# Kernel tuning notes

Measured on AMD Instinct MI355X. Metric: run time of the kernel, lower is better.

## Reference

```python
import jax, jax.numpy as jnp
import numpy as np

N_LIG, M_POC = 16384, 32768
E_LIG, E_POC, K_CROSS = 163840, 327680, 8
H = 64
L = 4

silu = jax.nn.silu


def _lin(k, fan_in, fan_out):
    k1, k2 = jax.random.split(k)
    s = 1.0 / np.sqrt(fan_in)
    W = jax.random.uniform(k1, (fan_in, fan_out), jnp.float32, -s, s)
    b = jax.random.uniform(k2, (fan_out,), jnp.float32, -s, s)
    return W, b


def setup_inputs() -> dict:
    key = jax.random.key(0)
    ks = jax.random.split(key, 32)
    inp = {
        'lig_x': jax.random.normal(ks[0], (N_LIG, 3), jnp.float32),
        'lig_h': jax.random.normal(ks[1], (N_LIG, 17), jnp.float32),
        'poc_x': jax.random.normal(ks[2], (M_POC, 3), jnp.float32),
        'poc_h': jax.random.normal(ks[3], (M_POC, 29), jnp.float32),
        'lig_edge_index': jax.random.randint(ks[4], (2, E_LIG), 0, N_LIG, jnp.int32),
        'lig_edge_attr': jax.random.normal(ks[5], (E_LIG, 6), jnp.float32),
        'poc_edge_index': jax.random.randint(ks[6], (2, E_POC), 0, M_POC, jnp.int32),
        'poc_edge_attr': jax.random.normal(ks[7], (E_POC, 16), jnp.float32),
        'cross_edge_index': jnp.stack([
            jax.random.randint(ks[8], (N_LIG * K_CROSS,), 0, M_POC, jnp.int32),
            jax.random.randint(ks[9], (N_LIG * K_CROSS,), 0, N_LIG, jnp.int32)]),
        'cross_edge_attr': jax.random.normal(ks[10], (N_LIG * K_CROSS, 16), jnp.float32),
        't': jax.random.uniform(ks[11], (1,), jnp.float32),
    }
    # embeddings
    inp['lig_emb_W'], inp['lig_emb_b'] = _lin(ks[12], 18, H)
    inp['poc_emb_W'], inp['poc_emb_b'] = _lin(ks[13], 29, H)
    inp['lig_ee_W'], inp['lig_ee_b'] = _lin(ks[14], 6, H)
    inp['poc_ee_W'], inp['poc_ee_b'] = _lin(ks[15], 16, H)
    inp['cross_ee_W'], inp['cross_ee_b'] = _lin(ks[16], 16, H)
    # per-layer params stacked along leading L axis
    def stack(kk, fan_in, fan_out):
        Ws, bs = zip(*[_lin(k, fan_in, fan_out) for k in jax.random.split(kk, L)])
        return jnp.stack(Ws), jnp.stack(bs)
    inp['phi_e_W1'], inp['phi_e_b1'] = stack(ks[17], 2 * H + 1 + H, H)
    inp['phi_e_W2'], inp['phi_e_b2'] = stack(ks[18], H, H)
    inp['phi_x_W1'], inp['phi_x_b1'] = stack(ks[19], H, H)
    inp['phi_x_W2'], inp['phi_x_b2'] = stack(ks[20], H, 1)
    inp['phi_h_W1'], inp['phi_h_b1'] = stack(ks[21], 2 * H, H)
    inp['phi_h_W2'], inp['phi_h_b2'] = stack(ks[22], H, H)
    inp['out_W1'], inp['out_b1'] = _lin(ks[23], H, H)
    inp['out_W2'], inp['out_b2'] = _lin(ks[24], H, 1)
    return inp


def _forward(lig_x, lig_h, poc_x, poc_h, lig_edge_attr, poc_edge_attr,
             cross_edge_attr, t,
             lig_emb_W, lig_emb_b, poc_emb_W, poc_emb_b,
             lig_ee_W, lig_ee_b, poc_ee_W, poc_ee_b, cross_ee_W, cross_ee_b,
             phi_e_W1, phi_e_b1, phi_e_W2, phi_e_b2,
             phi_x_W1, phi_x_b1, phi_x_W2, phi_x_b2,
             phi_h_W1, phi_h_b1, phi_h_W2, phi_h_b2,
             out_W1, out_b1, out_W2, out_b2,
             lig_edge_index, poc_edge_index, cross_edge_index):
    n_lig = lig_h.shape[0]
    n_tot = n_lig + poc_h.shape[0]
    t_feat = jnp.broadcast_to(t.reshape(1, 1), (n_lig, 1))
    h_lig = jnp.concatenate([lig_h, t_feat], -1) @ lig_emb_W + lig_emb_b
    h_poc = poc_h @ poc_emb_W + poc_emb_b
    h = jnp.concatenate([h_lig, h_poc], 0)          # [N, H]
    x = jnp.concatenate([lig_x, poc_x], 0)          # [N, 3]
    src = jnp.concatenate([lig_edge_index[0], poc_edge_index[0] + n_lig,
                           cross_edge_index[0] + n_lig])
    dst = jnp.concatenate([lig_edge_index[1], poc_edge_index[1] + n_lig,
                           cross_edge_index[1]])
    eattr = jnp.concatenate([
        lig_edge_attr @ lig_ee_W + lig_ee_b,
        poc_edge_attr @ poc_ee_W + poc_ee_b,
        cross_edge_attr @ cross_ee_W + cross_ee_b], 0)  # [E, H]
    # True = pocket => coords not updated
    update_mask = jnp.concatenate([
        jnp.ones((n_lig, 1), h.dtype), jnp.zeros((n_tot - n_lig, 1), h.dtype)], 0)
    for i in range(phi_e_W1.shape[0]):
        diff = x[src] - x[dst]                                    # [E, 3]
        dist = jnp.sum(diff * diff, -1, keepdims=True) / 100.0    # [E, 1]
        e_in = jnp.concatenate([h[src], h[dst], dist, eattr], -1) # [E, 2H+1+H]
        m = silu(silu(e_in @ phi_e_W1[i] + phi_e_b1[i]) @ phi_e_W2[i] + phi_e_b2[i])
        cw = jnp.tanh(silu(m @ phi_x_W1[i] + phi_x_b1[i]) @ phi_x_W2[i] + phi_x_b2[i])
        coord_agg = jax.ops.segment_sum(diff * cw, dst, num_segments=n_tot) * update_mask
        msg_agg = jax.ops.segment_sum(m, dst, num_segments=n_tot)
        h = h + silu(jnp.concatenate([h, msg_agg], -1) @ phi_h_W1[i] + phi_h_b1[i]) @ phi_h_W2[i] + phi_h_b2[i]
        x = x + coord_agg
    disp = x[:n_lig] - lig_x
    scale = silu(h[:n_lig] @ out_W1 + out_b1) @ out_W2 + out_b2
    return scale * disp


def reference(lig_x, lig_h, poc_x, poc_h, lig_edge_attr, poc_edge_attr,
              cross_edge_attr, t,
              lig_emb_W, lig_emb_b, poc_emb_W, poc_emb_b,
              lig_ee_W, lig_ee_b, poc_ee_W, poc_ee_b, cross_ee_W, cross_ee_b,
              phi_e_W1, phi_e_b1, phi_e_W2, phi_e_b2,
              phi_x_W1, phi_x_b1, phi_x_W2, phi_x_b2,
              phi_h_W1, phi_h_b1, phi_h_W2, phi_h_b2,
              out_W1, out_b1, out_W2, out_b2,
              lig_edge_index, poc_edge_index, cross_edge_index):
    return _forward(lig_x, lig_h, poc_x, poc_h, lig_edge_attr, poc_edge_attr,
                    cross_edge_attr, t,
                    lig_emb_W, lig_emb_b, poc_emb_W, poc_emb_b,
                    lig_ee_W, lig_ee_b, poc_ee_W, poc_ee_b, cross_ee_W, cross_ee_b,
                    phi_e_W1, phi_e_b1, phi_e_W2, phi_e_b2,
                    phi_x_W1, phi_x_b1, phi_x_W2, phi_x_b2,
                    phi_h_W1, phi_h_b1, phi_h_W2, phi_h_b2,
                    out_W1, out_b1, out_W2, out_b2,
                    lig_edge_index, poc_edge_index, cross_edge_index)
```

## Files before the change

### kernel.cpp

```cpp
#include <hip/hip_runtime.h>

#define N_LIG 16384
#define M_POC 32768
#define N_TOT (N_LIG + M_POC)
#define E_LIG 163840
#define E_POC 327680
#define E_CROSS (N_LIG * 8)
#define E_TOT (E_LIG + E_POC + E_CROSS)
#define TE 16

typedef __bf16 bf16_t;
typedef bf16_t bf16x8 __attribute__((ext_vector_type(8)));
typedef bf16_t bf16x4 __attribute__((ext_vector_type(4)));
typedef float f32x4 __attribute__((ext_vector_type(4)));

#define SM 72
#define EDGE_WAVE_BYTES (32 * SM * 2)

__device__ __forceinline__ float fast_rcp(float x) { return __builtin_amdgcn_rcpf(x); }
__device__ __forceinline__ float silu_f(float v) {
    return v * fast_rcp(1.0f + __expf(-v));
}
__device__ __forceinline__ float tanh_f(float v) {
    float a = fabsf(v);
    float t = __expf(-2.0f * a);
    float r = (1.0f - t) * fast_rcp(1.0f + t);
    return copysignf(r, v);
}

__device__ __forceinline__ void atomic_add_f32(float* p, float v) {
    __hip_atomic_fetch_add(p, v, __ATOMIC_RELAXED, __HIP_MEMORY_SCOPE_AGENT);
}

__device__ __forceinline__ void lds_fence() {
    asm volatile("s_waitcnt lgkmcnt(0)" ::: "memory");
}


__global__ void k_build_edges(const int* __restrict__ lig_ei, const int* __restrict__ poc_ei,
                              const int* __restrict__ cross_ei,
                              int* __restrict__ srcA, int* __restrict__ dstA,
                              int* __restrict__ cnt) {
    int e = blockIdx.x * blockDim.x + threadIdx.x;
    if (e >= E_TOT) return;
    int s, d;
    if (e < E_LIG) {
        s = lig_ei[e];
        d = lig_ei[E_LIG + e];
    } else if (e < E_LIG + E_POC) {
        int i = e - E_LIG;
        s = poc_ei[i] + N_LIG;
        d = poc_ei[E_POC + i] + N_LIG;
    } else {
        int i = e - E_LIG - E_POC;
        s = cross_ei[i] + N_LIG;
        d = cross_ei[E_CROSS + i];
    }
    srcA[e] = s;
    dstA[e] = d;
    atomicAdd(&cnt[d], 1);
}

__global__ __launch_bounds__(1024) void k_scan(const int* __restrict__ cnt,
                                               int* __restrict__ rowptr,
                                               int* __restrict__ cursor) {
    __shared__ int sums[1024];
    int tid = threadIdx.x;
    int local[48];
    int s = 0;
    for (int i = 0; i < 48; ++i) { local[i] = s; s += cnt[tid * 48 + i]; }
    sums[tid] = s;
    __syncthreads();
    for (int off = 1; off < 1024; off <<= 1) {
        int v = (tid >= off) ? sums[tid - off] : 0;
        __syncthreads();
        sums[tid] += v;
        __syncthreads();
    }
    int base = (tid == 0) ? 0 : sums[tid - 1];
    for (int i = 0; i < 48; ++i) {
        int v = base + local[i];
        int idx = tid * 48 + i;
        rowptr[idx] = v;
        cursor[idx] = v;
    }
    if (tid == 1023) rowptr[N_TOT] = sums[1023];
}

__global__ void k_scatter(const int* __restrict__ dstA, int* __restrict__ cursor,
                          int* __restrict__ sortedPos) {
    int e = blockIdx.x * blockDim.x + threadIdx.x;
    if (e < E_TOT) sortedPos[e] = atomicAdd(&cursor[dstA[e]], 1);
}

#define PK_G1   (12 * 5 * 4 * 64)
#define PK_G23  (4 * 4 * 4 * 64)
#define PK_WH   (4 * 24 * 64)
#define PK_BEFF (12 * 64)
#define PK_TOT  (PK_G1 + PK_G23 + PK_WH + PK_BEFF)

__global__ void k_pack_all(const float* __restrict__ phi_e_W1, const float* __restrict__ phi_e_b1,
                           const float* __restrict__ lig_ee_W, const float* __restrict__ lig_ee_b,
                           const float* __restrict__ poc_ee_W, const float* __restrict__ poc_ee_b,
                           const float* __restrict__ cross_ee_W, const float* __restrict__ cross_ee_b,
                           const float* __restrict__ phi_e_W2, const float* __restrict__ phi_x_W1,
                           const float* __restrict__ phi_h_W1, const float* __restrict__ phi_h_W2,
                           bf16_t* __restrict__ Bg1, bf16_t* __restrict__ Bg23,
                           bf16_t* __restrict__ WhP, float* __restrict__ beff) {
    int tid = blockIdx.x * blockDim.x + threadIdx.x;
    if (tid < PK_G1) {
        int lt = tid / 1280;
        int rem = tid - lt * 1280;
        int c = rem >> 8;
        int ft = (rem >> 6) & 3;
        int lane = rem & 63;
        int l = lt / 3, t = lt % 3;
        const float* W1l = phi_e_W1 + l * 193 * 64;
        const float* We; int K;
        if (t == 0) { We = lig_ee_W; K = 6; }
        else if (t == 1) { We = poc_ee_W; K = 16; }
        else { We = cross_ee_W; K = 16; }
        int col = ft * 16 + (lane & 15);
        int k0 = c * 32 + (lane >> 4) * 8;
        #pragma unroll
        for (int j = 0; j < 8; ++j) {
            int row = k0 + j;
            float v = 0.0f;
            if (row < 128) v = W1l[row * 64 + col];
            else if (row < 144) {
                int kk = row - 128;
                if (kk < K) {
                    float a = 0.0f;
                    for (int q = 0; q < 64; ++q) a = fmaf(We[kk * 64 + q], W1l[(129 + q) * 64 + col], a);
                    v = a;
                }
            } else if (row == 144) {
                v = W1l[128 * 64 + col];
            }
            Bg1[(size_t)tid * 8 + j] = (bf16_t)v;
        }
    } else if (tid < PK_G1 + PK_G23) {
        int u = tid - PK_G1;
        int lane = u & 63;
        int ft = (u >> 6) & 3;
        int c = (u >> 8) & 3;
        int l = u >> 10;
        const float* W = (c < 2) ? (phi_e_W2 + l * 4096) : (phi_x_W1 + l * 4096);
        int kb = (c & 1) * 32;
        int col = ft * 16 + (lane & 15);
        int k0 = kb + (lane >> 4) * 8;
        #pragma unroll
        for (int j = 0; j < 8; ++j)
            Bg23[(size_t)u * 8 + j] = (bf16_t)W[(k0 + j) * 64 + col];
    } else if (tid < PK_G1 + PK_G23 + PK_WH) {
        int u = tid - PK_G1 - PK_G23;
        int lane = u & 63;
        int frag = (u >> 6) % 24;
        int l = (u >> 6) / 24;
        const float* W; int kc, ft;
        if (frag < 16) { W = phi_h_W1 + l * 128 * 64; kc = frag >> 2; ft = frag & 3; }
        else           { W = phi_h_W2 + l * 64 * 64;  kc = (frag - 16) >> 2; ft = (frag - 16) & 3; }
        int col = ft * 16 + (lane & 15);
        int k0 = kc * 32 + (lane >> 4) * 8;
        #pragma unroll
        for (int j = 0; j < 8; ++j)
            WhP[(size_t)u * 8 + j] = (bf16_t)W[(k0 + j) * 64 + col];
    } else if (tid < PK_TOT) {
        int u = tid - PK_G1 - PK_G23 - PK_WH;
        int j = u & 63;
        int lt = u >> 6;
        int l = lt / 3, t = lt % 3;
        const float* W1l = phi_e_W1 + l * 193 * 64;
        const float* Be = (t == 0) ? lig_ee_b : ((t == 1) ? poc_ee_b : cross_ee_b);
        float v = phi_e_b1[l * 64 + j];
        for (int q = 0; q < 64; ++q) v = fmaf(Be[q], W1l[(129 + q) * 64 + j], v);
        beff[u] = v;
    }
}

__global__ void k_embed(const float* __restrict__ lig_x, const float* __restrict__ lig_h,
                        const float* __restrict__ poc_x, const float* __restrict__ poc_h,
                        const float* __restrict__ t,
                        const float* __restrict__ ligW, const float* __restrict__ ligB,
                        const float* __restrict__ pocW, const float* __restrict__ pocB,
                        float* __restrict__ h, bf16_t* __restrict__ hB, float* __restrict__ x4) {
    int gid = blockIdx.x * blockDim.x + threadIdx.x;
    int n = gid >> 6;
    int lane = gid & 63;
    if (n >= N_TOT) return;
    float a;
    if (n < N_LIG) {
        a = ligB[lane];
        #pragma unroll
        for (int k = 0; k < 17; ++k) a = fmaf(lig_h[n * 17 + k], ligW[k * 64 + lane], a);
        a = fmaf(t[0], ligW[17 * 64 + lane], a);
        if (lane < 4) x4[n * 4 + lane] = (lane < 3) ? lig_x[n * 3 + lane] : 0.0f;
    } else {
        int p = n - N_LIG;
        a = pocB[lane];
        #pragma unroll
        for (int k = 0; k < 29; ++k) a = fmaf(poc_h[p * 29 + k], pocW[k * 64 + lane], a);
        if (lane < 4) x4[n * 4 + lane] = (lane < 3) ? poc_x[p * 3 + lane] : 0.0f;
    }
    h[n * 64 + lane] = a;
    hB[n * 64 + lane] = (bf16_t)a;
}

__global__ __launch_bounds__(256, 4) void k_edge_mfma(
    const bf16_t* __restrict__ hB, const float* __restrict__ x4,
    const int* __restrict__ srcA, const int* __restrict__ dstA,
    const int* __restrict__ sortedPos,
    const float* __restrict__ lig_attr, const float* __restrict__ poc_attr,
    const float* __restrict__ cross_attr,
    const bf16_t* __restrict__ Bg1L,
    const float* __restrict__ beffL,
    const bf16_t* __restrict__ Bg23L,
    const float* __restrict__ b2, const float* __restrict__ bx1,
    const float* __restrict__ Wx2, const float* __restrict__ bx2,
    bf16_t* __restrict__ mBuf, float* __restrict__ coord_agg) {
    __shared__ __align__(16) char lds[4 * EDGE_WAVE_BYTES];
    const int lane = threadIdx.x & 63;
    const int wave = threadIdx.x >> 6;
    bf16_t* mT = (bf16_t*)(lds + wave * EDGE_WAVE_BYTES);
    const int base = (blockIdx.x * 4 + wave) * 32;

    int tt; const float* attrBase; int astride;
    if (base < E_LIG) { tt = 0; attrBase = lig_attr + (size_t)base * 6; astride = 6; }
    else if (base < E_LIG + E_POC) { tt = 1; attrBase = poc_attr + (size_t)(base - E_LIG) * 16; astride = 16; }
    else { tt = 2; attrBase = cross_attr + (size_t)(base - E_LIG - E_POC) * 16; astride = 16; }

    const int edge = lane & 15;
    const int kgrp = lane >> 4;
    const int mrow0 = kgrp * 4;
    const int e0 = base + edge;
    const int e1 = base + 16 + edge;
    const int sv0 = srcA[e0], sv1 = srcA[e1];
    const int dv0 = dstA[e0], dv1 = dstA[e1];
    const int sp0 = sortedPos[e0], sp1 = sortedPos[e1];

    bf16x8 hs0a = *(const bf16x8*)(hB + (size_t)sv0 * 64 + kgrp * 8);
    bf16x8 hs0b = *(const bf16x8*)(hB + (size_t)sv0 * 64 + 32 + kgrp * 8);
    bf16x8 hd0a = *(const bf16x8*)(hB + (size_t)dv0 * 64 + kgrp * 8);
    bf16x8 hd0b = *(const bf16x8*)(hB + (size_t)dv0 * 64 + 32 + kgrp * 8);
    bf16x8 hs1a = *(const bf16x8*)(hB + (size_t)sv1 * 64 + kgrp * 8);
    bf16x8 hs1b = *(const bf16x8*)(hB + (size_t)sv1 * 64 + 32 + kgrp * 8);
    bf16x8 hd1a = *(const bf16x8*)(hB + (size_t)dv1 * 64 + kgrp * 8);
    bf16x8 hd1b = *(const bf16x8*)(hB + (size_t)dv1 * 64 + 32 + kgrp * 8);

    const bf16_t Z = (bf16_t)0.0f;
    bf16x8 ex0 = {Z, Z, Z, Z, Z, Z, Z, Z};
    bf16x8 ex1 = {Z, Z, Z, Z, Z, Z, Z, Z};
    float d0s0 = 0.f, d1s0 = 0.f, d2s0 = 0.f;
    float d0s1 = 0.f, d1s1 = 0.f, d2s1 = 0.f;
    if (kgrp == 0) {
        const float* a0p = attrBase + (size_t)edge * astride;
        const float* a1p = attrBase + (size_t)(16 + edge) * astride;
        if (tt == 0) {
            float4 q0 = *(const float4*)a0p;
            float2 q1 = *(const float2*)(a0p + 4);
            ex0 = (bf16x8){(bf16_t)q0.x, (bf16_t)q0.y, (bf16_t)q0.z, (bf16_t)q0.w,
                           (bf16_t)q1.x, (bf16_t)q1.y, Z, Z};
            float4 r0 = *(const float4*)a1p;
            float2 r1 = *(const float2*)(a1p + 4);
            ex1 = (bf16x8){(bf16_t)r0.x, (bf16_t)r0.y, (bf16_t)r0.z, (bf16_t)r0.w,
                           (bf16_t)r1.x, (bf16_t)r1.y, Z, Z};
        } else {
            float4 q0 = *(const float4*)a0p;
            float4 q1 = *(const float4*)(a0p + 4);
            ex0 = (bf16x8){(bf16_t)q0.x, (bf16_t)q0.y, (bf16_t)q0.z, (bf16_t)q0.w,
                           (bf16_t)q1.x, (bf16_t)q1.y, (bf16_t)q1.z, (bf16_t)q1.w};
            float4 r0 = *(const float4*)a1p;
            float4 r1 = *(const float4*)(a1p + 4);
            ex1 = (bf16x8){(bf16_t)r0.x, (bf16_t)r0.y, (bf16_t)r0.z, (bf16_t)r0.w,
                           (bf16_t)r1.x, (bf16_t)r1.y, (bf16_t)r1.z, (bf16_t)r1.w};
        }
    } else if (kgrp == 1) {
        if (tt != 0) {
            const float* a0p = attrBase + (size_t)edge * astride + 8;
            const float* a1p = attrBase + (size_t)(16 + edge) * astride + 8;
            float4 q0 = *(const float4*)a0p;
            float4 q1 = *(const float4*)(a0p + 4);
            ex0 = (bf16x8){(bf16_t)q0.x, (bf16_t)q0.y, (bf16_t)q0.z, (bf16_t)q0.w,
                           (bf16_t)q1.x, (bf16_t)q1.y, (bf16_t)q1.z, (bf16_t)q1.w};
            float4 r0 = *(const float4*)a1p;
            float4 r1 = *(const float4*)(a1p + 4);
            ex1 = (bf16x8){(bf16_t)r0.x, (bf16_t)r0.y, (bf16_t)r0.z, (bf16_t)r0.w,
                           (bf16_t)r1.x, (bf16_t)r1.y, (bf16_t)r1.z, (bf16_t)r1.w};
        }
    } else if (kgrp == 2) {
        float4 xs0 = *(const float4*)(x4 + (size_t)sv0 * 4);
        float4 xd0 = *(const float4*)(x4 + (size_t)dv0 * 4);
        float4 xs1 = *(const float4*)(x4 + (size_t)sv1 * 4);
        float4 xd1 = *(const float4*)(x4 + (size_t)dv1 * 4);
        d0s0 = xs0.x - xd0.x; d1s0 = xs0.y - xd0.y; d2s0 = xs0.z - xd0.z;
        d0s1 = xs1.x - xd1.x; d1s1 = xs1.y - xd1.y; d2s1 = xs1.z - xd1.z;
        float dist0 = (d0s0 * d0s0 + d1s0 * d1s0 + d2s0 * d2s0) * 0.01f;
        float dist1 = (d0s1 * d0s1 + d1s1 * d1s1 + d2s1 * d2s1) * 0.01f;
        ex0[0] = (bf16_t)dist0;
        ex1[0] = (bf16_t)dist1;
    }

    const bf16_t* Bg1 = Bg1L + (size_t)tt * 5 * 4 * 512;
    const float* beff = beffL + tt * 64;
    f32x4 acc0[4], acc1[4];
    #pragma unroll
    for (int ft = 0; ft < 4; ++ft) {
        float4 bv = *(const float4*)(beff + ft * 16 + mrow0);
        acc0[ft] = (f32x4){bv.x, bv.y, bv.z, bv.w};
        acc1[ft] = acc0[ft];
    }
    bf16x8 bdat0[5] = {hs0a, hs0b, hd0a, hd0b, ex0};
    bf16x8 bdat1[5] = {hs1a, hs1b, hd1a, hd1b, ex1};
    #pragma unroll
    for (int c = 0; c < 5; ++c) {
        #pragma unroll
        for (int ft = 0; ft < 4; ++ft) {
            bf16x8 wfr = *(const bf16x8*)(Bg1 + ((size_t)(c * 4 + ft) * 64 + lane) * 8);
            acc0[ft] = __builtin_amdgcn_mfma_f32_16x16x32_bf16(wfr, bdat0[c], acc0[ft], 0, 0, 0);
            acc1[ft] = __builtin_amdgcn_mfma_f32_16x16x32_bf16(wfr, bdat1[c], acc1[ft], 0, 0, 0);
        }
    }
    #pragma unroll
    for (int ft = 0; ft < 4; ++ft) {
        bf16x4 v0 = {(bf16_t)silu_f(acc0[ft][0]), (bf16_t)silu_f(acc0[ft][1]),
                     (bf16_t)silu_f(acc0[ft][2]), (bf16_t)silu_f(acc0[ft][3])};
        bf16x4 v1 = {(bf16_t)silu_f(acc1[ft][0]), (bf16_t)silu_f(acc1[ft][1]),
                     (bf16_t)silu_f(acc1[ft][2]), (bf16_t)silu_f(acc1[ft][3])};
        *(bf16x4*)(mT + edge * SM + ft * 16 + mrow0) = v0;
        *(bf16x4*)(mT + (16 + edge) * SM + ft * 16 + mrow0) = v1;
    }
    lds_fence();

    f32x4 acc20[4], acc21[4];
    #pragma unroll
    for (int ft = 0; ft < 4; ++ft) {
        float4 bv = *(const float4*)(b2 + ft * 16 + mrow0);
        acc20[ft] = (f32x4){bv.x, bv.y, bv.z, bv.w};
        acc21[ft] = acc20[ft];
    }
    bf16x8 m10[2], m11[2];
    #pragma unroll
    for (int c = 0; c < 2; ++c) {
        m10[c] = *(const bf16x8*)(mT + edge * SM + c * 32 + kgrp * 8);
        m11[c] = *(const bf16x8*)(mT + (16 + edge) * SM + c * 32 + kgrp * 8);
    }
    #pragma unroll
    for (int c = 0; c < 2; ++c) {
        #pragma unroll
        for (int ft = 0; ft < 4; ++ft) {
            bf16x8 wfr = *(const bf16x8*)(Bg23L + ((size_t)(c * 4 + ft) * 64 + lane) * 8);
            acc20[ft] = __builtin_amdgcn_mfma_f32_16x16x32_bf16(wfr, m10[c], acc20[ft], 0, 0, 0);
            acc21[ft] = __builtin_amdgcn_mfma_f32_16x16x32_bf16(wfr, m11[c], acc21[ft], 0, 0, 0);
        }
    }
    lds_fence();
    #pragma unroll
    for (int ft = 0; ft < 4; ++ft) {
        bf16x4 v0 = {(bf16_t)silu_f(acc20[ft][0]), (bf16_t)silu_f(acc20[ft][1]),
                     (bf16_t)silu_f(acc20[ft][2]), (bf16_t)silu_f(acc20[ft][3])};
        bf16x4 v1 = {(bf16_t)silu_f(acc21[ft][0]), (bf16_t)silu_f(acc21[ft][1]),
                     (bf16_t)silu_f(acc21[ft][2]), (bf16_t)silu_f(acc21[ft][3])};
        *(bf16x4*)(mT + edge * SM + ft * 16 + mrow0) = v0;
        *(bf16x4*)(mT + (16 + edge) * SM + ft * 16 + mrow0) = v1;
    }
    lds_fence();

    bf16x8 g0[2], g1[2];
    #pragma unroll
    for (int c = 0; c < 2; ++c) {
        g0[c] = *(const bf16x8*)(mT + edge * SM + c * 32 + kgrp * 8);
        g1[c] = *(const bf16x8*)(mT + (16 + edge) * SM + c * 32 + kgrp * 8);
        *(bf16x8*)(mBuf + (size_t)sp0 * 64 + c * 32 + kgrp * 8) = g0[c];
        *(bf16x8*)(mBuf + (size_t)sp1 * 64 + c * 32 + kgrp * 8) = g1[c];
    }

    f32x4 acc30[4], acc31[4];
    #pragma unroll
    for (int ft = 0; ft < 4; ++ft) {
        float4 bv = *(const float4*)(bx1 + ft * 16 + mrow0);
        acc30[ft] = (f32x4){bv.x, bv.y, bv.z, bv.w};
        acc31[ft] = acc30[ft];
    }
    const bf16_t* Bg3 = Bg23L + (size_t)2 * 4 * 512;
    #pragma unroll
    for (int c = 0; c < 2; ++c) {
        #pragma unroll
        for (int ft = 0; ft < 4; ++ft) {
            bf16x8 wfr = *(const bf16x8*)(Bg3 + ((size_t)(c * 4 + ft) * 64 + lane) * 8);
            acc30[ft] = __builtin_amdgcn_mfma_f32_16x16x32_bf16(wfr, g0[c], acc30[ft], 0, 0, 0);
            acc31[ft] = __builtin_amdgcn_mfma_f32_16x16x32_bf16(wfr, g1[c], acc31[ft], 0, 0, 0);
        }
    }

    float s0 = 0.0f, s1 = 0.0f;
    #pragma unroll
    for (int ft = 0; ft < 4; ++ft) {
        float4 wv = *(const float4*)(Wx2 + ft * 16 + mrow0);
        s0 = fmaf(silu_f(acc30[ft][0]), wv.x, s0);
        s0 = fmaf(silu_f(acc30[ft][1]), wv.y, s0);
        s0 = fmaf(silu_f(acc30[ft][2]), wv.z, s0);
        s0 = fmaf(silu_f(acc30[ft][3]), wv.w, s0);
        s1 = fmaf(silu_f(acc31[ft][0]), wv.x, s1);
        s1 = fmaf(silu_f(acc31[ft][1]), wv.y, s1);
        s1 = fmaf(silu_f(acc31[ft][2]), wv.z, s1);
        s1 = fmaf(silu_f(acc31[ft][3]), wv.w, s1);
    }
    s0 += __shfl_xor(s0, 16, 64); s0 += __shfl_xor(s0, 32, 64);
    s1 += __shfl_xor(s1, 16, 64); s1 += __shfl_xor(s1, 32, 64);
    const float bx2v = bx2[0];
    const float cw0 = tanh_f(s0 + bx2v);
    const float cw1 = tanh_f(s1 + bx2v);

    float a0 = __shfl(d0s0, 32 + edge, 64);
    float a1 = __shfl(d1s0, 32 + edge, 64);
    float a2 = __shfl(d2s0, 32 + edge, 64);
    float b0 = __shfl(d0s1, 32 + edge, 64);
    float b1 = __shfl(d1s1, 32 + edge, 64);
    float b2v_ = __shfl(d2s1, 32 + edge, 64);
    if (kgrp < 3) {
        float dsel0 = (kgrp == 0) ? a0 : ((kgrp == 1) ? a1 : a2);
        float dsel1 = (kgrp == 0) ? b0 : ((kgrp == 1) ? b1 : b2v_);
        if (dv0 < N_LIG) atomic_add_f32(&coord_agg[dv0 * 3 + kgrp], dsel0 * cw0);
        if (dv1 < N_LIG) atomic_add_f32(&coord_agg[dv1 * 3 + kgrp], dsel1 * cw1);
    }
}

#define NODE_WAVE_BYTES (2304 + 2304)
__global__ __launch_bounds__(256) void k_node(
    float* __restrict__ h, bf16_t* __restrict__ hB, float* __restrict__ x4,
    const bf16_t* __restrict__ mBuf, const int* __restrict__ rowptr,
    float* __restrict__ coord,
    const bf16_t* __restrict__ WhL,
    const float* __restrict__ bh1, const float* __restrict__ bh2) {
    __shared__ __align__(16) char lds[4 * NODE_WAVE_BYTES];
    const int lane = threadIdx.x & 63;
    const int wave = threadIdx.x >> 6;
    bf16_t* msgT = (bf16_t*)(lds + wave * NODE_WAVE_BYTES);
    bf16_t* mid  = (bf16_t*)(lds + wave * NODE_WAVE_BYTES + 2304);
    const int base = (blockIdx.x * 4 + wave) * TE;

    const int node = lane & 15;
    const int kgrp = lane >> 4;
    const int mrow0 = kgrp * 4;
    const int n16 = base + node;

    const int rp0 = rowptr[n16];
    const int rp1 = rowptr[n16 + 1];
    const int f4 = node * 4;
    for (int r = 0; r < TE; ++r) {
        const int s0 = __shfl(rp0, r, 64);
        const int s1 = __shfl(rp1, r, 64);
        float a0 = 0.f, a1 = 0.f, a2 = 0.f, a3 = 0.f;
        for (int i = s0 + kgrp; i < s1; i += 4) {
            bf16x4 v = *(const bf16x4*)(mBuf + (size_t)i * 64 + f4);
            a0 += (float)v[0]; a1 += (float)v[1]; a2 += (float)v[2]; a3 += (float)v[3];
        }
        a0 += __shfl_xor(a0, 16, 64); a1 += __shfl_xor(a1, 16, 64);
        a2 += __shfl_xor(a2, 16, 64); a3 += __shfl_xor(a3, 16, 64);
        a0 += __shfl_xor(a0, 32, 64); a1 += __shfl_xor(a1, 32, 64);
        a2 += __shfl_xor(a2, 32, 64); a3 += __shfl_xor(a3, 32, 64);
        if (lane < 16) {
            bf16x4 v = {(bf16_t)a0, (bf16_t)a1, (bf16_t)a2, (bf16_t)a3};
            *(bf16x4*)(msgT + r * SM + f4) = v;
        }
    }
    lds_fence();

    f32x4 acc[4];
    #pragma unroll
    for (int ft = 0; ft < 4; ++ft) {
        float4 bv = *(const float4*)(bh1 + ft * 16 + mrow0);
        acc[ft] = (f32x4){bv.x, bv.y, bv.z, bv.w};
    }
    bf16x8 d0 = *(const bf16x8*)(hB + (size_t)n16 * 64 + kgrp * 8);
    bf16x8 d1 = *(const bf16x8*)(hB + (size_t)n16 * 64 + 32 + kgrp * 8);
    bf16x8 d2 = *(const bf16x8*)(msgT + node * SM + kgrp * 8);
    bf16x8 d3 = *(const bf16x8*)(msgT + node * SM + 32 + kgrp * 8);
    bf16x8 bdat[4] = {d0, d1, d2, d3};
    #pragma unroll
    for (int c = 0; c < 4; ++c) {
        #pragma unroll
        for (int ft = 0; ft < 4; ++ft) {
            bf16x8 wfr = *(const bf16x8*)(WhL + ((size_t)(c * 4 + ft) * 64 + lane) * 8);
            acc[ft] = __builtin_amdgcn_mfma_f32_16x16x32_bf16(wfr, bdat[c], acc[ft], 0, 0, 0);
        }
    }
    #pragma unroll
    for (int ft = 0; ft < 4; ++ft) {
        bf16x4 v = {(bf16_t)silu_f(acc[ft][0]), (bf16_t)silu_f(acc[ft][1]),
                    (bf16_t)silu_f(acc[ft][2]), (bf16_t)silu_f(acc[ft][3])};
        *(bf16x4*)(mid + node * SM + ft * 16 + mrow0) = v;
    }
    lds_fence();

    f32x4 acc2[4];
    #pragma unroll
    for (int ft = 0; ft < 4; ++ft) {
        float4 bv = *(const float4*)(bh2 + ft * 16 + mrow0);
        acc2[ft] = (f32x4){bv.x, bv.y, bv.z, bv.w};
    }
    bf16x8 g0 = *(const bf16x8*)(mid + node * SM + kgrp * 8);
    bf16x8 g1 = *(const bf16x8*)(mid + node * SM + 32 + kgrp * 8);
    #pragma unroll
    for (int c = 0; c < 2; ++c) {
        bf16x8 df = (c == 0) ? g0 : g1;
        #pragma unroll
        for (int ft = 0; ft < 4; ++ft) {
            bf16x8 wfr = *(const bf16x8*)(WhL + ((size_t)(16 + c * 4 + ft) * 64 + lane) * 8);
            acc2[ft] = __builtin_amdgcn_mfma_f32_16x16x32_bf16(wfr, df, acc2[ft], 0, 0, 0);
        }
    }

    #pragma unroll
    for (int ft = 0; ft < 4; ++ft) {
        float* hp = h + (size_t)n16 * 64 + ft * 16 + mrow0;
        float4 hv = *(const float4*)hp;
        hv.x += acc2[ft][0]; hv.y += acc2[ft][1]; hv.z += acc2[ft][2]; hv.w += acc2[ft][3];
        *(float4*)hp = hv;
        bf16x4 hb = {(bf16_t)hv.x, (bf16_t)hv.y, (bf16_t)hv.z, (bf16_t)hv.w};
        *(bf16x4*)(hB + (size_t)n16 * 64 + ft * 16 + mrow0) = hb;
    }
    if (kgrp < 3) {
        if (n16 < N_LIG) x4[n16 * 4 + kgrp] += coord[n16 * 3 + kgrp];
        coord[n16 * 3 + kgrp] = 0.0f;
    }
}

__global__ void k_out(const float* __restrict__ h, const float* __restrict__ x4,
                      const float* __restrict__ lig_x,
                      const float* __restrict__ oW1, const float* __restrict__ ob1,
                      const float* __restrict__ oW2, const float* __restrict__ ob2,
                      float* __restrict__ out) {
    int gid = blockIdx.x * blockDim.x + threadIdx.x;
    int n = gid >> 6;
    int lane = gid & 63;
    if (n >= N_LIG) return;
    float hv = h[n * 64 + lane];
    float a = ob1[lane];
    #pragma unroll
    for (int k = 0; k < 64; ++k) a = fmaf(__shfl(hv, k, 64), oW1[k * 64 + lane], a);
    float p = silu_f(a) * oW2[lane];
    #pragma unroll
    for (int off = 32; off > 0; off >>= 1) p += __shfl_xor(p, off, 64);
    float scale = p + ob2[0];
    if (lane < 3) out[n * 3 + lane] = scale * (x4[n * 4 + lane] - lig_x[n * 3 + lane]);
}

extern "C" void kernel_launch(void* const* d_in, const int* in_sizes, int n_in,
                              void* d_out, int out_size, void* d_ws, size_t ws_size,
                              hipStream_t stream) {
    const float* lig_x      = (const float*)d_in[0];
    const float* lig_h      = (const float*)d_in[1];
    const float* poc_x      = (const float*)d_in[2];
    const float* poc_h      = (const float*)d_in[3];
    const int*   lig_ei     = (const int*)d_in[4];
    const float* lig_attr   = (const float*)d_in[5];
    const int*   poc_ei     = (const int*)d_in[6];
    const float* poc_attr   = (const float*)d_in[7];
    const int*   cross_ei   = (const int*)d_in[8];
    const float* cross_attr = (const float*)d_in[9];
    const float* t          = (const float*)d_in[10];
    const float* lig_emb_W  = (const float*)d_in[11];
    const float* lig_emb_b  = (const float*)d_in[12];
    const float* poc_emb_W  = (const float*)d_in[13];
    const float* poc_emb_b  = (const float*)d_in[14];
    const float* lig_ee_W   = (const float*)d_in[15];
    const float* lig_ee_b   = (const float*)d_in[16];
    const float* poc_ee_W   = (const float*)d_in[17];
    const float* poc_ee_b   = (const float*)d_in[18];
    const float* cross_ee_W = (const float*)d_in[19];
    const float* cross_ee_b = (const float*)d_in[20];
    const float* phi_e_W1   = (const float*)d_in[21];
    const float* phi_e_b1   = (const float*)d_in[22];
    const float* phi_e_W2   = (const float*)d_in[23];
    const float* phi_e_b2   = (const float*)d_in[24];
    const float* phi_x_W1   = (const float*)d_in[25];
    const float* phi_x_b1   = (const float*)d_in[26];
    const float* phi_x_W2   = (const float*)d_in[27];
    const float* phi_x_b2   = (const float*)d_in[28];
    const float* phi_h_W1   = (const float*)d_in[29];
    const float* phi_h_b1   = (const float*)d_in[30];
    const float* phi_h_W2   = (const float*)d_in[31];
    const float* phi_h_b2   = (const float*)d_in[32];
    const float* out_W1     = (const float*)d_in[33];
    const float* out_b1     = (const float*)d_in[34];
    const float* out_W2     = (const float*)d_in[35];
    const float* out_b2     = (const float*)d_in[36];

    char* p = (char*)d_ws;
    auto carve = [&](size_t bytes) { char* r = p; p += (bytes + 255) & ~(size_t)255; return r; };
    float*  h      = (float*)carve((size_t)N_TOT * 64 * 4);
    bf16_t* hB     = (bf16_t*)carve((size_t)N_TOT * 64 * 2);
    float*  x4     = (float*)carve((size_t)N_TOT * 4 * 4);
    float*  coord  = (float*)carve((size_t)N_TOT * 3 * 4);
    bf16_t* WhP    = (bf16_t*)carve((size_t)4 * 24 * 512 * 2);
    float*  beff   = (float*)carve((size_t)12 * 64 * 4);
    bf16_t* Bg1    = (bf16_t*)carve((size_t)12 * 5 * 4 * 512 * 2);
    bf16_t* Bg23   = (bf16_t*)carve((size_t)4 * 16 * 512 * 2);
    int*    srcA   = (int*)carve((size_t)E_TOT * 4);
    int*    dstA   = (int*)carve((size_t)E_TOT * 4);
    int*    sortedPos = (int*)carve((size_t)E_TOT * 4);
    int*    cnt    = (int*)carve((size_t)N_TOT * 4);
    int*    cursor = (int*)carve((size_t)N_TOT * 4);
    int*    rowptr = (int*)carve((size_t)(N_TOT + 1) * 4);
    bf16_t* mBuf   = (bf16_t*)carve((size_t)E_TOT * 64 * 2);

    hipMemsetAsync(cnt, 0, (size_t)N_TOT * 4, stream);
    hipMemsetAsync(coord, 0, (size_t)N_TOT * 3 * 4, stream);
    k_build_edges<<<E_TOT / 256, 256, 0, stream>>>(lig_ei, poc_ei, cross_ei, srcA, dstA, cnt);
    k_scan<<<1, 1024, 0, stream>>>(cnt, rowptr, cursor);
    k_scatter<<<E_TOT / 256, 256, 0, stream>>>(dstA, cursor, sortedPos);
    k_pack_all<<<(PK_TOT + 255) / 256, 256, 0, stream>>>(
        phi_e_W1, phi_e_b1, lig_ee_W, lig_ee_b, poc_ee_W, poc_ee_b, cross_ee_W, cross_ee_b,
        phi_e_W2, phi_x_W1, phi_h_W1, phi_h_W2, Bg1, Bg23, WhP, beff);
    k_embed<<<(N_TOT * 64) / 256, 256, 0, stream>>>(
        lig_x, lig_h, poc_x, poc_h, t, lig_emb_W, lig_emb_b, poc_emb_W, poc_emb_b, h, hB, x4);

    for (int l = 0; l < 4; ++l) {
        k_edge_mfma<<<E_TOT / 128, 256, 0, stream>>>(
            hB, x4, srcA, dstA, sortedPos, lig_attr, poc_attr, cross_attr,
            Bg1 + (size_t)l * 3 * 5 * 4 * 512, beff + (size_t)l * 3 * 64,
            Bg23 + (size_t)l * 16 * 512,
            phi_e_b2 + l * 64, phi_x_b1 + l * 64,
            phi_x_W2 + l * 64, phi_x_b2 + l,
            mBuf, coord);
        k_node<<<N_TOT / 64, 256, 0, stream>>>(
            h, hB, x4, mBuf, rowptr, coord,
            WhP + (size_t)l * 24 * 512,
            phi_h_b1 + l * 64, phi_h_b2 + l * 64);
    }

    k_out<<<(N_LIG * 64) / 256, 256, 0, stream>>>(
        h, x4, lig_x, out_W1, out_b1, out_W2, out_b2, (float*)d_out);
}
```

Baseline: 748.1 us.

## Split node message aggregation into separate gather kernel and prepack edge attributes to bf16

Moves the per-node CSR sum of edge messages out of k_node into a new k_gather kernel. It runs one wave per 4 nodes, so far more waves work on the gather than in the old 16-nodes-per-wave loop, and it writes the aggregated messages to a global bf16 buffer that k_node then reads. Separately, edge attributes from the three edge types are packed once into a uniform 16-wide bf16 array, so the edge kernel loads them with a single vector load instead of branching on type and converting from fp32 every layer. The cost is an extra kernel launch and global round trip per layer, plus one extra packing pass and buffer.

```diff
diff --git a/kernel.cpp b/kernel.cpp
--- a/kernel.cpp
+++ b/kernel.cpp
@@ -59,6 +59,19 @@
     srcA[e] = s;
     dstA[e] = d;
     atomicAdd(&cnt[d], 1);
+}
+
+__global__ void k_pack_attr(const float* __restrict__ lig_attr, const float* __restrict__ poc_attr,
+                            const float* __restrict__ cross_attr, bf16_t* __restrict__ attrF) {
+    int e = blockIdx.x * blockDim.x + threadIdx.x;
+    if (e >= E_TOT) return;
+    const float* a; int K;
+    if (e < E_LIG) { a = lig_attr + (size_t)e * 6; K = 6; }
+    else if (e < E_LIG + E_POC) { a = poc_attr + (size_t)(e - E_LIG) * 16; K = 16; }
+    else { a = cross_attr + (size_t)(e - E_LIG - E_POC) * 16; K = 16; }
+    bf16_t* o = attrF + (size_t)e * 16;
+    #pragma unroll
+    for (int k = 0; k < 16; ++k) o[k] = (bf16_t)((k < K) ? a[k] : 0.0f);
 }
 
 __global__ __launch_bounds__(1024) void k_scan(const int* __restrict__ cnt,
@@ -210,8 +223,7 @@
     const bf16_t* __restrict__ hB, const float* __restrict__ x4,
     const int* __restrict__ srcA, const int* __restrict__ dstA,
     const int* __restrict__ sortedPos,
-    const float* __restrict__ lig_attr, const float* __restrict__ poc_attr,
-    const float* __restrict__ cross_attr,
+    const bf16_t* __restrict__ attrF,
     const bf16_t* __restrict__ Bg1L,
     const float* __restrict__ beffL,
     const bf16_t* __restrict__ Bg23L,
@@ -224,10 +236,10 @@
     bf16_t* mT = (bf16_t*)(lds + wave * EDGE_WAVE_BYTES);
     const int base = (blockIdx.x * 4 + wave) * 32;
 
-    int tt; const float* attrBase; int astride;
-    if (base < E_LIG) { tt = 0; attrBase = lig_attr + (size_t)base * 6; astride = 6; }
-    else if (base < E_LIG + E_POC) { tt = 1; attrBase = poc_attr + (size_t)(base - E_LIG) * 16; astride = 16; }
-    else { tt = 2; attrBase = cross_attr + (size_t)(base - E_LIG - E_POC) * 16; astride = 16; }
+    int tt;
+    if (base < E_LIG) tt = 0;
+    else if (base < E_LIG + E_POC) tt = 1;
+    else tt = 2;
 
     const int edge = lane & 15;
     const int kgrp = lane >> 4;
@@ -252,41 +264,9 @@
     bf16x8 ex1 = {Z, Z, Z, Z, Z, Z, Z, Z};
     float d0s0 = 0.f, d1s0 = 0.f, d2s0 = 0.f;
     float d0s1 = 0.f, d1s1 = 0.f, d2s1 = 0.f;
-    if (kgrp == 0) {
-        const float* a0p = attrBase + (size_t)edge * astride;
-        const float* a1p = attrBase + (size_t)(16 + edge) * astride;
-        if (tt == 0) {
-            float4 q0 = *(const float4*)a0p;
-            float2 q1 = *(const float2*)(a0p + 4);
-            ex0 = (bf16x8){(bf16_t)q0.x, (bf16_t)q0.y, (bf16_t)q0.z, (bf16_t)q0.w,
-                           (bf16_t)q1.x, (bf16_t)q1.y, Z, Z};
-            float4 r0 = *(const float4*)a1p;
-            float2 r1 = *(const float2*)(a1p + 4);
-            ex1 = (bf16x8){(bf16_t)r0.x, (bf16_t)r0.y, (bf16_t)r0.z, (bf16_t)r0.w,
-                           (bf16_t)r1.x, (bf16_t)r1.y, Z, Z};
-        } else {
-            float4 q0 = *(const float4*)a0p;
-            float4 q1 = *(const float4*)(a0p + 4);
-            ex0 = (bf16x8){(bf16_t)q0.x, (bf16_t)q0.y, (bf16_t)q0.z, (bf16_t)q0.w,
-                           (bf16_t)q1.x, (bf16_t)q1.y, (bf16_t)q1.z, (bf16_t)q1.w};
-            float4 r0 = *(const float4*)a1p;
-            float4 r1 = *(const float4*)(a1p + 4);
-            ex1 = (bf16x8){(bf16_t)r0.x, (bf16_t)r0.y, (bf16_t)r0.z, (bf16_t)r0.w,
-                           (bf16_t)r1.x, (bf16_t)r1.y, (bf16_t)r1.z, (bf16_t)r1.w};
-        }
-    } else if (kgrp == 1) {
-        if (tt != 0) {
-            const float* a0p = attrBase + (size_t)edge * astride + 8;
-            const float* a1p = attrBase + (size_t)(16 + edge) * astride + 8;
-            float4 q0 = *(const float4*)a0p;
-            float4 q1 = *(const float4*)(a0p + 4);
-            ex0 = (bf16x8){(bf16_t)q0.x, (bf16_t)q0.y, (bf16_t)q0.z, (bf16_t)q0.w,
-                           (bf16_t)q1.x, (bf16_t)q1.y, (bf16_t)q1.z, (bf16_t)q1.w};
-            float4 r0 = *(const float4*)a1p;
-            float4 r1 = *(const float4*)(a1p + 4);
-            ex1 = (bf16x8){(bf16_t)r0.x, (bf16_t)r0.y, (bf16_t)r0.z, (bf16_t)r0.w,
-                           (bf16_t)r1.x, (bf16_t)r1.y, (bf16_t)r1.z, (bf16_t)r1.w};
-        }
+    if (kgrp < 2) {
+        ex0 = *(const bf16x8*)(attrF + (size_t)e0 * 16 + kgrp * 8);
+        ex1 = *(const bf16x8*)(attrF + (size_t)e1 * 16 + kgrp * 8);
     } else if (kgrp == 2) {
         float4 xs0 = *(const float4*)(x4 + (size_t)sv0 * 4);
         float4 xd0 = *(const float4*)(x4 + (size_t)dv0 * 4);
@@ -425,18 +405,46 @@
     }
 }
 
-#define NODE_WAVE_BYTES (2304 + 2304)
+__global__ __launch_bounds__(256) void k_gather(
+    const bf16_t* __restrict__ mBuf, const int* __restrict__ rowptr,
+    bf16_t* __restrict__ msgB) {
+    const int lane = threadIdx.x & 63;
+    const int wave = threadIdx.x >> 6;
+    const int fq = lane & 15;
+    const int sub = lane >> 4;
+    const int nbase = (blockIdx.x * 4 + wave) * 4;
+    #pragma unroll
+    for (int r = 0; r < 4; ++r) {
+        const int n = nbase + r;
+        const int s0 = rowptr[n];
+        const int s1 = rowptr[n + 1];
+        float a0 = 0.f, a1 = 0.f, a2 = 0.f, a3 = 0.f;
+        for (int i = s0 + sub; i < s1; i += 4) {
+            bf16x4 v = *(const bf16x4*)(mBuf + (size_t)i * 64 + fq * 4);
+            a0 += (float)v[0]; a1 += (float)v[1]; a2 += (float)v[2]; a3 += (float)v[3];
+        }
+        a0 += __shfl_xor(a0, 16, 64); a1 += __shfl_xor(a1, 16, 64);
+        a2 += __shfl_xor(a2, 16, 64); a3 += __shfl_xor(a3, 16, 64);
+        a0 += __shfl_xor(a0, 32, 64); a1 += __shfl_xor(a1, 32, 64);
+        a2 += __shfl_xor(a2, 32, 64); a3 += __shfl_xor(a3, 32, 64);
+        if (lane < 16) {
+            bf16x4 v = {(bf16_t)a0, (bf16_t)a1, (bf16_t)a2, (bf16_t)a3};
+            *(bf16x4*)(msgB + (size_t)n * 64 + fq * 4) = v;
+        }
+    }
+}
+
+#define NODE_WAVE_BYTES 2304
 __global__ __launch_bounds__(256) void k_node(
     float* __restrict__ h, bf16_t* __restrict__ hB, float* __restrict__ x4,
-    const bf16_t* __restrict__ mBuf, const int* __restrict__ rowptr,
+    const bf16_t* __restrict__ msgB,
     float* __restrict__ coord,
     const bf16_t* __restrict__ WhL,
     const float* __restrict__ bh1, const float* __restrict__ bh2) {
     __shared__ __align__(16) char lds[4 * NODE_WAVE_BYTES];
     const int lane = threadIdx.x & 63;
     const int wave = threadIdx.x >> 6;
-    bf16_t* msgT = (bf16_t*)(lds + wave * NODE_WAVE_BYTES);
-    bf16_t* mid  = (bf16_t*)(lds + wave * NODE_WAVE_BYTES + 2304);
+    bf16_t* mid = (bf16_t*)(lds + wave * NODE_WAVE_BYTES);
     const int base = (blockIdx.x * 4 + wave) * TE;
 
     const int node = lane & 15;
@@ -444,28 +452,6 @@
     const int mrow0 = kgrp * 4;
     const int n16 = base + node;
 
-    const int rp0 = rowptr[n16];
-    const int rp1 = rowptr[n16 + 1];
-    const int f4 = node * 4;
-    for (int r = 0; r < TE; ++r) {
-        const int s0 = __shfl(rp0, r, 64);
-        const int s1 = __shfl(rp1, r, 64);
-        float a0 = 0.f, a1 = 0.f, a2 = 0.f, a3 = 0.f;
-        for (int i = s0 + kgrp; i < s1; i += 4) {
-            bf16x4 v = *(const bf16x4*)(mBuf + (size_t)i * 64 + f4);
-            a0 += (float)v[0]; a1 += (float)v[1]; a2 += (float)v[2]; a3 += (float)v[3];
-        }
-        a0 += __shfl_xor(a0, 16, 64); a1 += __shfl_xor(a1, 16, 64);
-        a2 += __shfl_xor(a2, 16, 64); a3 += __shfl_xor(a3, 16, 64);
-        a0 += __shfl_xor(a0, 32, 64); a1 += __shfl_xor(a1, 32, 64);
-        a2 += __shfl_xor(a2, 32, 64); a3 += __shfl_xor(a3, 32, 64);
-        if (lane < 16) {
-            bf16x4 v = {(bf16_t)a0, (bf16_t)a1, (bf16_t)a2, (bf16_t)a3};
-            *(bf16x4*)(msgT + r * SM + f4) = v;
-        }
-    }
-    lds_fence();
-
     f32x4 acc[4];
     #pragma unroll
     for (int ft = 0; ft < 4; ++ft) {
@@ -474,8 +460,8 @@
     }
     bf16x8 d0 = *(const bf16x8*)(hB + (size_t)n16 * 64 + kgrp * 8);
     bf16x8 d1 = *(const bf16x8*)(hB + (size_t)n16 * 64 + 32 + kgrp * 8);
-    bf16x8 d2 = *(const bf16x8*)(msgT + node * SM + kgrp * 8);
-    bf16x8 d3 = *(const bf16x8*)(msgT + node * SM + 32 + kgrp * 8);
+    bf16x8 d2 = *(const bf16x8*)(msgB + (size_t)n16 * 64 + kgrp * 8);
+    bf16x8 d3 = *(const bf16x8*)(msgB + (size_t)n16 * 64 + 32 + kgrp * 8);
     bf16x8 bdat[4] = {d0, d1, d2, d3};
     #pragma unroll
     for (int c = 0; c < 4; ++c) {
@@ -591,12 +577,14 @@
     auto carve = [&](size_t bytes) { char* r = p; p += (bytes + 255) & ~(size_t)255; return r; };
     float*  h      = (float*)carve((size_t)N_TOT * 64 * 4);
     bf16_t* hB     = (bf16_t*)carve((size_t)N_TOT * 64 * 2);
+    bf16_t* msgB   = (bf16_t*)carve((size_t)N_TOT * 64 * 2);
     float*  x4     = (float*)carve((size_t)N_TOT * 4 * 4);
     float*  coord  = (float*)carve((size_t)N_TOT * 3 * 4);
     bf16_t* WhP    = (bf16_t*)carve((size_t)4 * 24 * 512 * 2);
     float*  beff   = (float*)carve((size_t)12 * 64 * 4);
     bf16_t* Bg1    = (bf16_t*)carve((size_t)12 * 5 * 4 * 512 * 2);
     bf16_t* Bg23   = (bf16_t*)carve((size_t)4 * 16 * 512 * 2);
+    bf16_t* attrF  = (bf16_t*)carve((size_t)E_TOT * 16 * 2);
     int*    srcA   = (int*)carve((size_t)E_TOT * 4);
     int*    dstA   = (int*)carve((size_t)E_TOT * 4);
     int*    sortedPos = (int*)carve((size_t)E_TOT * 4);
@@ -608,6 +596,7 @@
     hipMemsetAsync(cnt, 0, (size_t)N_TOT * 4, stream);
     hipMemsetAsync(coord, 0, (size_t)N_TOT * 3 * 4, stream);
     k_build_edges<<<E_TOT / 256, 256, 0, stream>>>(lig_ei, poc_ei, cross_ei, srcA, dstA, cnt);
+    k_pack_attr<<<E_TOT / 256, 256, 0, stream>>>(lig_attr, poc_attr, cross_attr, attrF);
     k_scan<<<1, 1024, 0, stream>>>(cnt, rowptr, cursor);
     k_scatter<<<E_TOT / 256, 256, 0, stream>>>(dstA, cursor, sortedPos);
     k_pack_all<<<(PK_TOT + 255) / 256, 256, 0, stream>>>(
@@ -618,14 +607,15 @@
 
     for (int l = 0; l < 4; ++l) {
         k_edge_mfma<<<E_TOT / 128, 256, 0, stream>>>(
-            hB, x4, srcA, dstA, sortedPos, lig_attr, poc_attr, cross_attr,
+            hB, x4, srcA, dstA, sortedPos, attrF,
             Bg1 + (size_t)l * 3 * 5 * 4 * 512, beff + (size_t)l * 3 * 64,
             Bg23 + (size_t)l * 16 * 512,
             phi_e_b2 + l * 64, phi_x_b1 + l * 64,
             phi_x_W2 + l * 64, phi_x_b2 + l,
             mBuf, coord);
+        k_gather<<<N_TOT / 16, 256, 0, stream>>>(mBuf, rowptr, msgB);
         k_node<<<N_TOT / 64, 256, 0, stream>>>(
-            h, hB, x4, mBuf, rowptr, coord,
+            h, hB, x4, msgB, coord,
             WhP + (size_t)l * 24 * 512,
             phi_h_b1 + l * 64, phi_h_b2 + l * 64);
     }
```

New measurement: 721.2 us. -3.6%, faster.
